# Kernel tuning notes

Hardware: AMD Instinct MI355X
Metric: run time of the kernel (lower is better)

## Reference

```python
import jax, jax.numpy as jnp
import numpy as np

B, S, E, H = 4, 2048, 1024, 16
HD = E // H  # head_dim = 64


def setup_inputs() -> dict:
    key = jax.random.key(0)
    k1, k2, k3, k4 = jax.random.split(key, 4)
    x = jax.random.normal(k1, (B, S, E), dtype=jnp.float32)
    Wqkv = jax.random.normal(k2, (3 * E, E), dtype=jnp.float32) * (E ** -0.5)
    Wo = jax.random.normal(k3, (E, E), dtype=jnp.float32) * (E ** -0.5)
    bo = jax.random.normal(k4, (E,), dtype=jnp.float32) * 0.01
    return {"x": x, "Wqkv": Wqkv, "Wo": Wo, "bo": bo}


def reference(x, Wqkv, Wo, bo):
    b, s, e = x.shape
    # qkv projection (nn.Linear without bias: x @ W^T) -> (b, s, 3e)
    qkv = x @ Wqkv.T
    # reshape (b, s, H, 3*HD) -> (b, H, s, 3*HD), then chunk into q,k,v
    qkv = qkv.reshape(b, s, H, 3 * HD).transpose(0, 2, 1, 3)
    q, k, v = jnp.split(qkv, 3, axis=-1)  # each (b, H, s, HD)
    scale = 1.0 / jnp.sqrt(jnp.asarray(HD, dtype=x.dtype))
    scores = jnp.einsum('bhqd,bhkd->bhqk', q, k) * scale  # (b, H, s, s)
    causal = jnp.tril(jnp.ones((s, s), dtype=bool))
    scores = jnp.where(causal, scores, -jnp.inf)
    probs = jax.nn.softmax(scores, axis=-1)
    out = jnp.einsum('bhqk,bhkd->bhqd', probs, v)  # (b, H, s, HD)
    out = out.transpose(0, 2, 1, 3).reshape(b, s, e)
    return out @ Wo.T + bo
```

## Files before the change

kernel.cpp:

```cpp
#include <hip/hip_runtime.h>
#include <stdint.h>

#define Bn 4
#define Sn 2048
#define En 1024
#define Hn 16
#define HDn 64

typedef __bf16 bf16;
typedef __bf16 bf16x4 __attribute__((ext_vector_type(4)));
typedef __bf16 bf16x8 __attribute__((ext_vector_type(8)));
typedef float  f32x4  __attribute__((ext_vector_type(4)));
typedef float  f32x16 __attribute__((ext_vector_type(16)));
typedef uint32_t u32x4 __attribute__((ext_vector_type(4)));
typedef int      i32x2 __attribute__((ext_vector_type(2)));

#define GLDS(gp, lp) __builtin_amdgcn_global_load_lds( \
    (const __attribute__((address_space(1))) void*)(gp), \
    (__attribute__((address_space(3))) void*)(lp), 16, 0, 0)

#define BAR() __builtin_amdgcn_s_barrier()
#define WLG() do { asm volatile("s_waitcnt lgkmcnt(0)" ::: "memory"); \
                   __builtin_amdgcn_sched_barrier(0); } while (0)
#define WVM4() asm volatile("s_waitcnt vmcnt(4)" ::: "memory")

static __device__ __forceinline__ i32x2 plsw(uint32_t a, uint32_t b)
{
    return __builtin_amdgcn_permlane32_swap((int)a, (int)b, false, false);
}

__global__ __launch_bounds__(256) void cvt_f32_to_bf16(
    const float* __restrict__ in, bf16* __restrict__ out, int n4)
{
    int i = blockIdx.x * 256 + threadIdx.x;
    if (i >= n4) return;
    float4 f = reinterpret_cast<const float4*>(in)[i];
    bf16x4 o;
    o[0] = (bf16)f.x; o[1] = (bf16)f.y; o[2] = (bf16)f.z; o[3] = (bf16)f.w;
    reinterpret_cast<bf16x4*>(out)[i] = o;
}

template<int MODE>
__global__ __launch_bounds__(512, 2) void gemm256(
    const bf16* __restrict__ Ag, const bf16* __restrict__ Bw,
    int M, int N, int K,
    bf16* __restrict__ q_out, bf16* __restrict__ k_out, bf16* __restrict__ v_out,
    float* __restrict__ c_out, const float* __restrict__ bias)
{
    __shared__ __align__(16) bf16 lA[2 * 256 * 64];
    __shared__ __align__(16) bf16 lB[2 * 256 * 64];

    const int tid  = threadIdx.x;
    const int lane = tid & 63;
    const int w    = tid >> 6;
    const int wm = w >> 2, wn = w & 3;
    const int lr = lane & 15, lg = lane >> 4;
    const int m0 = blockIdx.y * 256;
    const int n0 = blockIdx.x * 256;
    const int NT = K >> 6;
    const int niter = NT >> 1;

    const int srow = tid >> 3;
    const int sck  = (tid & 7) ^ ((tid >> 3) & 7);

    f32x4 acc[8][4] = {};

    auto stageA = [&](int t, int half) {
        const int ts = t < NT ? t : NT - 1;
        bf16* Ld = lA + ((t & 1) ? 16384 : 0) + (half*128 + w*8) * 64;
        const bf16* S = Ag + (size_t)(m0 + half*128 + srow) * K + ts*64 + sck*8;
        GLDS(S, Ld);
        GLDS(S + (size_t)64 * K, Ld + 64 * 64);
    };
    auto stageB = [&](int t, int half) {
        const int ts = t < NT ? t : NT - 1;
        bf16* Ld = lB + ((t & 1) ? 16384 : 0) + (half*128 + w*8) * 64;
        const bf16* S = Bw + (size_t)(n0 + half*128 + srow) * K + ts*64 + sck*8;
        GLDS(S, Ld);
        GLDS(S + (size_t)64 * K, Ld + 64 * 64);
    };
    auto ldA4 = [&](bf16x8 (&a)[4][2], const bf16* Lb, int qm) {
        #pragma unroll
        for (int ii = 0; ii < 4; ++ii) {
            const bf16* p = Lb + (wm*128 + qm*64 + ii*16 + lr) * 64;
            #pragma unroll
            for (int kk = 0; kk < 2; ++kk)
                a[ii][kk] = *reinterpret_cast<const bf16x8*>(p + (((kk << 2) + lg) ^ (lr & 7)) * 8);
        }
    };
    auto ldB2 = [&](bf16x8 (&b)[2][2], const bf16* Lb, int qn) {
        #pragma unroll
        for (int j = 0; j < 2; ++j) {
            const bf16* p = Lb + (wn*64 + qn*32 + j*16 + lr) * 64;
            #pragma unroll
            for (int kk = 0; kk < 2; ++kk)
                b[j][kk] = *reinterpret_cast<const bf16x8*>(p + (((kk << 2) + lg) ^ (lr & 7)) * 8);
        }
    };
    auto mmac = [&](const bf16x8 (&a)[4][2], const bf16x8 (&b)[2][2], int qm, int qn) {
        __builtin_amdgcn_s_setprio(1);
        #pragma unroll
        for (int ii = 0; ii < 4; ++ii)
            #pragma unroll
            for (int j = 0; j < 2; ++j)
                #pragma unroll
                for (int kk = 0; kk < 2; ++kk)
                    acc[qm*4 + ii][qn*2 + j] = __builtin_amdgcn_mfma_f32_16x16x32_bf16(
                        a[ii][kk], b[j][kk], acc[qm*4 + ii][qn*2 + j], 0, 0, 0);
        __builtin_amdgcn_s_setprio(0);
    };

    stageA(0, 0); stageA(0, 1); stageB(0, 0); stageB(0, 1);
    stageB(1, 0); stageB(1, 1);
    WVM4(); BAR();

    const bf16* A0 = lA;          const bf16* A1 = lA + 16384;
    const bf16* B0l = lB;         const bf16* B1l = lB + 16384;
    bf16x8 a[4][2], b0[2][2], b1[2][2];

    for (int i = 0; i < niter; ++i) {
        const int t = 2 * i;
        ldA4(a, A0, 0); ldB2(b0, B0l, 0);
        stageA(t + 1, 0);
        BAR(); WLG();
        mmac(a, b0, 0, 0);
        BAR();
        ldB2(b1, B0l, 1);
        stageA(t + 1, 1);
        BAR(); WLG();
        mmac(a, b1, 0, 1);
        BAR();
        ldA4(a, A0, 1);
        stageB(t + 2, 0);
        BAR(); WLG();
        mmac(a, b0, 1, 0);
        BAR();
        stageB(t + 2, 1);
        WVM4(); BAR();
        mmac(a, b1, 1, 1);
        BAR();
        ldA4(a, A1, 0); ldB2(b0, B1l, 0);
        stageA(t + 2, 0);
        BAR(); WLG();
        mmac(a, b0, 0, 0);
        BAR();
        ldB2(b1, B1l, 1);
        stageA(t + 2, 1);
        BAR(); WLG();
        mmac(a, b1, 0, 1);
        BAR();
        ldA4(a, A1, 1);
        stageB(t + 3, 0);
        BAR(); WLG();
        mmac(a, b0, 1, 0);
        BAR();
        stageB(t + 3, 1);
        WVM4(); BAR();
        mmac(a, b1, 1, 1);
        BAR();
    }

    #pragma unroll
    for (int ii = 0; ii < 8; ++ii) {
        #pragma unroll
        for (int j = 0; j < 4; ++j) {
            const int colb = n0 + wn*64 + j*16 + lr;
            #pragma unroll
            for (int r = 0; r < 4; ++r) {
                const int rowb = m0 + wm*128 + ii*16 + lg*4 + r;
                const float v = acc[ii][j][r];
                if (MODE == 0) {
                    const int bb = rowb >> 11, s = rowb & (Sn - 1);
                    const int h = colb / 192, rr = colb - h*192;
                    const int wq = rr >> 6, hd = rr & 63;
                    const size_t off = (((size_t)(bb*Hn + h))*Sn + s)*HDn + hd;
                    const bf16 bv = (bf16)v;
                    if (wq == 0)      q_out[off] = bv;
                    else if (wq == 1) k_out[off] = bv;
                    else              v_out[off] = bv;
                } else {
                    c_out[(size_t)rowb*N + colb] = v + bias[colb];
                }
            }
        }
    }
}

__global__ __launch_bounds__(256) void gemm_bt(
    const bf16* __restrict__ A, const bf16* __restrict__ Bw,
    int M, int N, int K,
    float* __restrict__ c_out, const float* __restrict__ bias)
{
    __shared__ bf16 lA[128*64];
    __shared__ bf16 lB[128*64];
    const int tid  = threadIdx.x;
    const int lane = tid & 63;
    const int wv   = tid >> 6;
    const int wm = wv >> 1, wn = wv & 1;
    const int m0 = blockIdx.y * 128;
    const int n0 = blockIdx.x * 128;
    const int lr = lane & 15, lg = lane >> 4;

    f32x4 acc[4][4] = {};

    const int rowA = wv*8 + (lane>>3);
    const int col8 = (lane&7)*8;

    for (int k0 = 0; k0 < K; k0 += 64) {
        #pragma unroll
        for (int c = 0; c < 4; ++c) {
            int row = c*32 + rowA;
            GLDS(A  + (size_t)(m0+row)*K + k0 + col8, lA + (c*32 + wv*8)*64);
            GLDS(Bw + (size_t)(n0+row)*K + k0 + col8, lB + (c*32 + wv*8)*64);
        }
        __syncthreads();
        #pragma unroll
        for (int kk = 0; kk < 64; kk += 32) {
            bf16x8 af[4], bfv[4];
            #pragma unroll
            for (int i = 0; i < 4; ++i)
                af[i] = *reinterpret_cast<const bf16x8*>(lA + (wm*64 + i*16 + lr)*64 + kk + lg*8);
            #pragma unroll
            for (int j = 0; j < 4; ++j)
                bfv[j] = *reinterpret_cast<const bf16x8*>(lB + (wn*64 + j*16 + lr)*64 + kk + lg*8);
            #pragma unroll
            for (int i = 0; i < 4; ++i)
                #pragma unroll
                for (int j = 0; j < 4; ++j)
                    acc[i][j] = __builtin_amdgcn_mfma_f32_16x16x32_bf16(af[i], bfv[j], acc[i][j], 0, 0, 0);
        }
        __syncthreads();
    }

    #pragma unroll
    for (int i = 0; i < 4; ++i) {
        #pragma unroll
        for (int j = 0; j < 4; ++j) {
            const int colb = n0 + wn*64 + j*16 + lr;
            #pragma unroll
            for (int r = 0; r < 4; ++r) {
                const int rowb = m0 + wm*64 + i*16 + lg*4 + r;
                c_out[(size_t)rowb*N + colb] = acc[i][j][r] + bias[colb];
            }
        }
    }
}

static __device__ __forceinline__ uint32_t pkbf(float lo, float hi)
{
    uint16_t a = __builtin_bit_cast(uint16_t, (bf16)lo);
    uint16_t b = __builtin_bit_cast(uint16_t, (bf16)hi);
    return (uint32_t)a | ((uint32_t)b << 16);
}

__global__ __launch_bounds__(512) void attn_fwd(
    const bf16* __restrict__ Q, const bf16* __restrict__ Kg, const bf16* __restrict__ Vg,
    bf16* __restrict__ O)
{
    __shared__ __align__(16) bf16 Kl[2][64*64];
    __shared__ __align__(16) bf16 Vt[2][64*64];

    const int tid  = threadIdx.x;
    const int lane = tid & 63;
    const int w    = tid >> 6;
    const int col  = lane & 31;
    const int hv   = lane >> 5;
    const int bh   = blockIdx.x;
    const int qb   = (gridDim.y - 1) - blockIdx.y;
    const int q0w  = qb*256 + w*32;
    const int qg   = q0w + col;

    const bf16* Qb = Q  + (size_t)bh*Sn*HDn;
    const bf16* Kb = Kg + (size_t)bh*Sn*HDn;
    const bf16* Vb = Vg + (size_t)bh*Sn*HDn;

    bf16x8 aq[4];
    #pragma unroll
    for (int ks = 0; ks < 4; ++ks)
        aq[ks] = *reinterpret_cast<const bf16x8*>(Qb + (size_t)qg*HDn + ks*16 + hv*8);

    f32x16 ov[2] = {};
    const float S2 = 0.18033688011112042f;
    float l_run = 0.f;

    const int skey = tid >> 3;
    const int scc  = tid & 7;
    const int ksw  = scc ^ (skey & 7);

    const int nst = 2*(qb+1);
    for (int sti = 0; sti < nst; ++sti) {
        const int k0 = sti*128;
        __syncthreads();
        GLDS(Kb + (size_t)(k0 + skey)*HDn + ksw*8,      &Kl[0][0] + (size_t)w*512);
        GLDS(Kb + (size_t)(k0 + 64 + skey)*HDn + ksw*8, &Kl[1][0] + (size_t)w*512);
        {
            bf16x8 v0 = *reinterpret_cast<const bf16x8*>(Vb + (size_t)(k0 + skey)*HDn + scc*8);
            bf16x8 v1 = *reinterpret_cast<const bf16x8*>(Vb + (size_t)(k0 + 64 + skey)*HDn + scc*8);
            #pragma unroll
            for (int j = 0; j < 8; ++j) {
                const int chunk = (scc*8 + j)*8 + ((skey>>3) ^ scc);
                Vt[0][chunk*8 + (skey&7)] = v0[j];
                Vt[1][chunk*8 + (skey&7)] = v1[j];
            }
        }
        __syncthreads();

        #pragma unroll
        for (int sub = 0; sub < 2; ++sub) {
            const int k0s = k0 + sub*64;
            if (k0s > q0w + 31) continue;

            f32x16 st[2] = {};
            #pragma unroll
            for (int kb = 0; kb < 2; ++kb) {
                const int key = kb*32 + col;
                #pragma unroll
                for (int ks = 0; ks < 4; ++ks) {
                    const int chunk = key*8 + ((ks*2 + hv) ^ (key & 7));
                    bf16x8 kf = *reinterpret_cast<const bf16x8*>(&Kl[sub][0] + chunk*8);
                    st[kb] = __builtin_amdgcn_mfma_f32_32x32x16_bf16(kf, aq[ks], st[kb], 0, 0, 0);
                }
            }

            if (k0s + 63 > q0w) {
                #pragma unroll
                for (int kb = 0; kb < 2; ++kb)
                    #pragma unroll
                    for (int r = 0; r < 16; ++r) {
                        const int keyg = k0s + kb*32 + (r&3) + 8*(r>>2) + 4*hv;
                        if (keyg > qg) st[kb][r] = -1e30f;
                    }
            }

            uint32_t wpk[2][8];
            float lsum = 0.f;
            #pragma unroll
            for (int kb = 0; kb < 2; ++kb) {
                float pr[8];
                #pragma unroll
                for (int i = 0; i < 8; ++i) {
                    const float e0 = exp2f(fmaf(st[kb][2*i],   S2, -8.0f));
                    const float e1 = exp2f(fmaf(st[kb][2*i+1], S2, -8.0f));
                    pr[i] = e0 + e1;
                    wpk[kb][i] = pkbf(e0, e1);
                }
                pr[0] += pr[4]; pr[1] += pr[5]; pr[2] += pr[6]; pr[3] += pr[7];
                pr[0] += pr[2]; pr[1] += pr[3];
                lsum += pr[0] + pr[1];
            }
            l_run += lsum;

            bf16x8 pB[4];
            #pragma unroll
            for (int s = 0; s < 4; ++s) {
                const int kb = s >> 1, ls = s & 1;
                i32x2 r02 = plsw(wpk[kb][4*ls+0], wpk[kb][4*ls+2]);
                i32x2 r13 = plsw(wpk[kb][4*ls+1], wpk[kb][4*ls+3]);
                u32x4 pwv = { (uint32_t)r02[0], (uint32_t)r13[0],
                              (uint32_t)r02[1], (uint32_t)r13[1] };
                pB[s] = __builtin_bit_cast(bf16x8, pwv);
            }

            #pragma unroll
            for (int s = 0; s < 4; ++s) {
                #pragma unroll
                for (int hb = 0; hb < 2; ++hb) {
                    const int hd = hb*32 + col;
                    const int chunk = hd*8 + ((s*2 + hv) ^ ((hd>>3) & 7));
                    bf16x8 vf = *reinterpret_cast<const bf16x8*>(&Vt[sub][0] + chunk*8);
                    ov[hb] = __builtin_amdgcn_mfma_f32_32x32x16_bf16(vf, pB[s], ov[hb], 0, 0, 0);
                }
            }
        }
    }

    const float lt  = l_run + __shfl_xor(l_run, 32);
    const float inv = 1.0f / lt;
    const int b = bh >> 4, hh = bh & 15;
    bf16* Ob = O + ((size_t)(b*Sn + qg))*En + hh*HDn;
    #pragma unroll
    for (int hb = 0; hb < 2; ++hb)
        #pragma unroll
        for (int g = 0; g < 4; ++g) {
            bf16x4 o4;
            #pragma unroll
            for (int r4 = 0; r4 < 4; ++r4)
                o4[r4] = (bf16)(ov[hb][g*4 + r4] * inv);
            *reinterpret_cast<bf16x4*>(Ob + hb*32 + g*8 + 4*hv) = o4;
        }
}

extern "C" void kernel_launch(void* const* d_in, const int* in_sizes, int n_in,
                              void* d_out, int out_size, void* d_ws, size_t ws_size,
                              hipStream_t stream)
{
    (void)in_sizes; (void)n_in; (void)out_size; (void)ws_size;
    const float* x    = (const float*)d_in[0];
    const float* Wqkv = (const float*)d_in[1];
    const float* Wo   = (const float*)d_in[2];
    const float* bo   = (const float*)d_in[3];
    float* out = (float*)d_out;

    const size_t nBS = (size_t)Bn*Sn;
    char* ws = (char*)d_ws;
    bf16* xb    = (bf16*)ws; ws += nBS*En*2;
    bf16* wqkvb = (bf16*)ws; ws += (size_t)3*En*En*2;
    bf16* wob   = (bf16*)ws; ws += (size_t)En*En*2;
    bf16* Qb    = (bf16*)ws; ws += nBS*En*2;
    bf16* Kb    = (bf16*)ws; ws += nBS*En*2;
    bf16* Vb    = (bf16*)ws; ws += nBS*En*2;
    bf16* AO    = (bf16*)ws; ws += nBS*En*2;

    int n4 = (int)(nBS*En/4);
    cvt_f32_to_bf16<<<(n4+255)/256, 256, 0, stream>>>(x, xb, n4);
    n4 = 3*En*En/4;
    cvt_f32_to_bf16<<<(n4+255)/256, 256, 0, stream>>>(Wqkv, wqkvb, n4);
    n4 = En*En/4;
    cvt_f32_to_bf16<<<(n4+255)/256, 256, 0, stream>>>(Wo, wob, n4);

    gemm256<0><<<dim3(3*En/256, nBS/256), 512, 0, stream>>>(
        xb, wqkvb, (int)nBS, 3*En, En, Qb, Kb, Vb, nullptr, nullptr);

    attn_fwd<<<dim3(Bn*Hn, Sn/256), 512, 0, stream>>>(Qb, Kb, Vb, AO);

    gemm_bt<<<dim3(En/128, nBS/128), 256, 0, stream>>>(
        AO, wob, (int)nBS, En, En, out, bo);
}
```

Before: 186.9 us.

## Pair causal query blocks per workgroup to balance attention work

Each attention workgroup now handles two 256-row query blocks, p and 7-p, so every block does equal causal work. The K/V tiles staged in LDS are shared by both query sets, which halves how often each K/V tile is reloaded. The grid drops from 512 to 256 workgroups, and each thread holds two Q fragment sets and two output accumulators. That raises register pressure and may lower occupancy, and the fewer, longer blocks may fill the GPU less evenly.

```diff
diff --git a/kernel.cpp b/kernel.cpp
--- a/kernel.cpp
+++ b/kernel.cpp
@@ -265,29 +265,95 @@
     const int w    = tid >> 6;
     const int col  = lane & 31;
     const int hv   = lane >> 5;
-    const int bh   = blockIdx.x;
-    const int qb   = (gridDim.y - 1) - blockIdx.y;
-    const int q0w  = qb*256 + w*32;
-    const int qg   = q0w + col;
+    const int bx   = blockIdx.x;
+    const int bh   = bx >> 2;
+    const int p    = bx & 3;
+    const int q0A  = p*256 + w*32;
+    const int q0B  = (7 - p)*256 + w*32;
+    const int qgA  = q0A + col;
+    const int qgB  = q0B + col;
 
     const bf16* Qb = Q  + (size_t)bh*Sn*HDn;
     const bf16* Kb = Kg + (size_t)bh*Sn*HDn;
     const bf16* Vb = Vg + (size_t)bh*Sn*HDn;
 
-    bf16x8 aq[4];
+    bf16x8 aqA[4], aqB[4];
     #pragma unroll
-    for (int ks = 0; ks < 4; ++ks)
-        aq[ks] = *reinterpret_cast<const bf16x8*>(Qb + (size_t)qg*HDn + ks*16 + hv*8);
-
-    f32x16 ov[2] = {};
+    for (int ks = 0; ks < 4; ++ks) {
+        aqA[ks] = *reinterpret_cast<const bf16x8*>(Qb + (size_t)qgA*HDn + ks*16 + hv*8);
+        aqB[ks] = *reinterpret_cast<const bf16x8*>(Qb + (size_t)qgB*HDn + ks*16 + hv*8);
+    }
+
+    f32x16 ovA[2] = {}, ovB[2] = {};
+    float lrA = 0.f, lrB = 0.f;
     const float S2 = 0.18033688011112042f;
-    float l_run = 0.f;
 
     const int skey = tid >> 3;
     const int scc  = tid & 7;
     const int ksw  = scc ^ (skey & 7);
 
-    const int nst = 2*(qb+1);
+    auto tileDo = [&](int k0s, int sub, int q0t, int qgt,
+                      bf16x8 (&aq)[4], f32x16 (&ov)[2], float& lr) {
+        f32x16 st[2] = {};
+        #pragma unroll
+        for (int kb = 0; kb < 2; ++kb) {
+            const int key = kb*32 + col;
+            #pragma unroll
+            for (int ks = 0; ks < 4; ++ks) {
+                const int chunk = key*8 + ((ks*2 + hv) ^ (key & 7));
+                bf16x8 kf = *reinterpret_cast<const bf16x8*>(&Kl[sub][0] + chunk*8);
+                st[kb] = __builtin_amdgcn_mfma_f32_32x32x16_bf16(kf, aq[ks], st[kb], 0, 0, 0);
+            }
+        }
+        if (k0s + 63 > q0t) {
+            #pragma unroll
+            for (int kb = 0; kb < 2; ++kb)
+                #pragma unroll
+                for (int r = 0; r < 16; ++r) {
+                    const int keyg = k0s + kb*32 + (r&3) + 8*(r>>2) + 4*hv;
+                    if (keyg > qgt) st[kb][r] = -1e30f;
+                }
+        }
+        uint32_t wpk[2][8];
+        float lsum = 0.f;
+        #pragma unroll
+        for (int kb = 0; kb < 2; ++kb) {
+            float pr[8];
+            #pragma unroll
+            for (int i = 0; i < 8; ++i) {
+                const float e0 = exp2f(fmaf(st[kb][2*i],   S2, -8.0f));
+                const float e1 = exp2f(fmaf(st[kb][2*i+1], S2, -8.0f));
+                pr[i] = e0 + e1;
+                wpk[kb][i] = pkbf(e0, e1);
+            }
+            pr[0] += pr[4]; pr[1] += pr[5]; pr[2] += pr[6]; pr[3] += pr[7];
+            pr[0] += pr[2]; pr[1] += pr[3];
+            lsum += pr[0] + pr[1];
+        }
+        lr += lsum;
+        bf16x8 pB[4];
+        #pragma unroll
+        for (int s = 0; s < 4; ++s) {
+            const int kb = s >> 1, ls = s & 1;
+            i32x2 r02 = plsw(wpk[kb][4*ls+0], wpk[kb][4*ls+2]);
+            i32x2 r13 = plsw(wpk[kb][4*ls+1], wpk[kb][4*ls+3]);
+            u32x4 pwv = { (uint32_t)r02[0], (uint32_t)r13[0],
+                          (uint32_t)r02[1], (uint32_t)r13[1] };
+            pB[s] = __builtin_bit_cast(bf16x8, pwv);
+        }
+        #pragma unroll
+        for (int s = 0; s < 4; ++s) {
+            #pragma unroll
+            for (int hb = 0; hb < 2; ++hb) {
+                const int hd = hb*32 + col;
+                const int chunk = hd*8 + ((s*2 + hv) ^ ((hd>>3) & 7));
+                bf16x8 vf = *reinterpret_cast<const bf16x8*>(&Vt[sub][0] + chunk*8);
+                ov[hb] = __builtin_amdgcn_mfma_f32_32x32x16_bf16(vf, pB[s], ov[hb], 0, 0, 0);
+            }
+        }
+    };
+
+    const int nst = 2*(8 - p);
     for (int sti = 0; sti < nst; ++sti) {
         const int k0 = sti*128;
         __syncthreads();
@@ -308,86 +374,29 @@
         #pragma unroll
         for (int sub = 0; sub < 2; ++sub) {
             const int k0s = k0 + sub*64;
-            if (k0s > q0w + 31) continue;
-
-            f32x16 st[2] = {};
-            #pragma unroll
-            for (int kb = 0; kb < 2; ++kb) {
-                const int key = kb*32 + col;
+            if (k0s <= q0A + 31) tileDo(k0s, sub, q0A, qgA, aqA, ovA, lrA);
+            if (k0s <= q0B + 31) tileDo(k0s, sub, q0B, qgB, aqB, ovB, lrB);
+        }
+    }
+
+    const int b = bh >> 4, hh = bh & 15;
+    auto epi = [&](int qgt, f32x16 (&ov)[2], float lr) {
+        const float lt  = lr + __shfl_xor(lr, 32);
+        const float inv = 1.0f / lt;
+        bf16* Ob = O + ((size_t)(b*Sn + qgt))*En + hh*HDn;
+        #pragma unroll
+        for (int hb = 0; hb < 2; ++hb)
+            #pragma unroll
+            for (int g = 0; g < 4; ++g) {
+                bf16x4 o4;
                 #pragma unroll
-                for (int ks = 0; ks < 4; ++ks) {
-                    const int chunk = key*8 + ((ks*2 + hv) ^ (key & 7));
-                    bf16x8 kf = *reinterpret_cast<const bf16x8*>(&Kl[sub][0] + chunk*8);
-                    st[kb] = __builtin_amdgcn_mfma_f32_32x32x16_bf16(kf, aq[ks], st[kb], 0, 0, 0);
-                }
-            }
-
-            if (k0s + 63 > q0w) {
-                #pragma unroll
-                for (int kb = 0; kb < 2; ++kb)
-                    #pragma unroll
-                    for (int r = 0; r < 16; ++r) {
-                        const int keyg = k0s + kb*32 + (r&3) + 8*(r>>2) + 4*hv;
-                        if (keyg > qg) st[kb][r] = -1e30f;
-                    }
-            }
-
-            uint32_t wpk[2][8];
-            float lsum = 0.f;
-            #pragma unroll
-            for (int kb = 0; kb < 2; ++kb) {
-                float pr[8];
-                #pragma unroll
-                for (int i = 0; i < 8; ++i) {
-                    const float e0 = exp2f(fmaf(st[kb][2*i],   S2, -8.0f));
-                    const float e1 = exp2f(fmaf(st[kb][2*i+1], S2, -8.0f));
-                    pr[i] = e0 + e1;
-                    wpk[kb][i] = pkbf(e0, e1);
-                }
-                pr[0] += pr[4]; pr[1] += pr[5]; pr[2] += pr[6]; pr[3] += pr[7];
-                pr[0] += pr[2]; pr[1] += pr[3];
-                lsum += pr[0] + pr[1];
-            }
-            l_run += lsum;
-
-            bf16x8 pB[4];
-            #pragma unroll
-            for (int s = 0; s < 4; ++s) {
-                const int kb = s >> 1, ls = s & 1;
-                i32x2 r02 = plsw(wpk[kb][4*ls+0], wpk[kb][4*ls+2]);
-                i32x2 r13 = plsw(wpk[kb][4*ls+1], wpk[kb][4*ls+3]);
-                u32x4 pwv = { (uint32_t)r02[0], (uint32_t)r13[0],
-                              (uint32_t)r02[1], (uint32_t)r13[1] };
-                pB[s] = __builtin_bit_cast(bf16x8, pwv);
-            }
-
-            #pragma unroll
-            for (int s = 0; s < 4; ++s) {
-                #pragma unroll
-                for (int hb = 0; hb < 2; ++hb) {
-                    const int hd = hb*32 + col;
-                    const int chunk = hd*8 + ((s*2 + hv) ^ ((hd>>3) & 7));
-                    bf16x8 vf = *reinterpret_cast<const bf16x8*>(&Vt[sub][0] + chunk*8);
-                    ov[hb] = __builtin_amdgcn_mfma_f32_32x32x16_bf16(vf, pB[s], ov[hb], 0, 0, 0);
-                }
-            }
-        }
-    }
-
-    const float lt  = l_run + __shfl_xor(l_run, 32);
-    const float inv = 1.0f / lt;
-    const int b = bh >> 4, hh = bh & 15;
-    bf16* Ob = O + ((size_t)(b*Sn + qg))*En + hh*HDn;
-    #pragma unroll
-    for (int hb = 0; hb < 2; ++hb)
-        #pragma unroll
-        for (int g = 0; g < 4; ++g) {
-            bf16x4 o4;
-            #pragma unroll
-            for (int r4 = 0; r4 < 4; ++r4)
-                o4[r4] = (bf16)(ov[hb][g*4 + r4] * inv);
-            *reinterpret_cast<bf16x4*>(Ob + hb*32 + g*8 + 4*hv) = o4;
-        }
+                for (int r4 = 0; r4 < 4; ++r4)
+                    o4[r4] = (bf16)(ov[hb][g*4 + r4] * inv);
+                *reinterpret_cast<bf16x4*>(Ob + hb*32 + g*8 + 4*hv) = o4;
+            }
+    };
+    epi(qgA, ovA, lrA);
+    epi(qgB, ovB, lrB);
 }
 
 extern "C" void kernel_launch(void* const* d_in, const int* in_sizes, int n_in,
@@ -421,7 +430,7 @@
     gemm256<0><<<dim3(3*En/256, nBS/256), 512, 0, stream>>>(
         xb, wqkvb, (int)nBS, 3*En, En, Qb, Kb, Vb, nullptr, nullptr);
 
-    attn_fwd<<<dim3(Bn*Hn, Sn/256), 512, 0, stream>>>(Qb, Kb, Vb, AO);
+    attn_fwd<<<dim3(Bn*Hn*4), 512, 0, stream>>>(Qb, Kb, Vb, AO);
 
     gemm_bt<<<dim3(En/128, nBS/128), 256, 0, stream>>>(
         AO, wob, (int)nBS, En, En, out, bo);
```

Measured after the change: 188.7 us. Within noise of the previous version (+1.0%).
